# Optimization experiments

Measured on AMD Instinct MI355X. Metric: run time of the kernel, lower is better.

The kernel has to match this reference:

```python
import jax, jax.numpy as jnp
import numpy as np

D_MODEL = 1024
D_FF = 4096
NUM_EXPERTS = 8
TOP_K = 2


def setup_inputs() -> dict:
    key = jax.random.key(0)
    ks = jax.random.split(key, 8)
    s_in = 1.0 / np.sqrt(D_MODEL)
    s_ff = 1.0 / np.sqrt(D_FF)
    x = jax.random.normal(ks[0], (2, 2048, D_MODEL), dtype=jnp.float32)
    Wg = jax.random.uniform(ks[1], (D_MODEL, NUM_EXPERTS), minval=-s_in, maxval=s_in, dtype=jnp.float32)
    bg = jax.random.uniform(ks[2], (NUM_EXPERTS,), minval=-s_in, maxval=s_in, dtype=jnp.float32)
    W1 = jax.random.uniform(ks[3], (NUM_EXPERTS, D_MODEL, D_FF), minval=-s_in, maxval=s_in, dtype=jnp.float32)
    b1 = jax.random.uniform(ks[4], (NUM_EXPERTS, D_FF), minval=-s_in, maxval=s_in, dtype=jnp.float32)
    W2 = jax.random.uniform(ks[5], (NUM_EXPERTS, D_FF, D_MODEL), minval=-s_ff, maxval=s_ff, dtype=jnp.float32)
    b2 = jax.random.uniform(ks[6], (NUM_EXPERTS, D_MODEL), minval=-s_ff, maxval=s_ff, dtype=jnp.float32)
    return {"x": x, "Wg": Wg, "bg": bg, "W1": W1, "b1": b1, "W2": W2, "b2": b2}


def reference(x, Wg, bg, W1, b1, W2, b2):
    # Gating: softmax over experts, top-k, renormalize
    gate_logits = jnp.einsum('bsd,de->bse', x, Wg) + bg
    gate_probs = jax.nn.softmax(gate_logits, axis=-1)
    topk_probs, topk_idx = jax.lax.top_k(gate_probs, TOP_K)
    topk_probs = topk_probs / jnp.sum(topk_probs, axis=-1, keepdims=True)
    # Per-token combine weights over experts [B,S,E] (top-k indices are unique)
    onehot = jax.nn.one_hot(topk_idx, NUM_EXPERTS, dtype=x.dtype)  # [B,S,K,E]
    weights = jnp.einsum('bske,bsk->bse', onehot, topk_probs)
    # Dense per-expert FFN (exact GELU matches torch nn.GELU default)
    h = jnp.einsum('bsd,edf->bsef', x, W1) + b1  # [B,S,E,Dff]
    h = jax.nn.gelu(h, approximate=False)
    y = jnp.einsum('bsef,efd->bsed', h, W2) + b2  # [B,S,E,D]
    return jnp.einsum('bsed,bse->bsd', y, weights)
```

## Files before the change

### kernel.cpp

```cpp
#include <hip/hip_runtime.h>
#include <hip/hip_bf16.h>
#include <math.h>

#define D_MODEL 1024
#define D_FF    4096
#define NE      8
#define NTOK    4096
#define MAXTOK  4096

#define MAXROWS 10240
#define MAXMT   40

typedef __attribute__((ext_vector_type(8))) short short8;
typedef __attribute__((ext_vector_type(4))) float f32x4;

#define WS_CNT     0
#define WS_OFFA    128
#define WS_TOKIDS  1024
#define WS_TOKW    (WS_TOKIDS + NE*MAXTOK*4)
#define WS_ROWTOK  (WS_TOKW + NE*MAXTOK*4)
#define WS_ROWW    (WS_ROWTOK + MAXROWS*4)
#define WS_TOKEXP  (WS_ROWW + MAXROWS*4)

#define WS_H       524288
#define WS_W1T     (WS_H   + (size_t)MAXROWS*D_FF*2)
#define WS_XG      (WS_W1T + (size_t)NE*D_MODEL*D_FF*2)
#define WS_W2T     (WS_XG  + (size_t)MAXROWS*D_MODEL*2)
#define WS_NEED_A  (WS_W2T + (size_t)NE*D_MODEL*D_FF*2)

__device__ __forceinline__ ushort f2b(float v) {
    __hip_bfloat16 b = __float2bfloat16(v);
    return *reinterpret_cast<ushort*>(&b);
}

__device__ __forceinline__ float gelu_f(float v) {
    float z = fabsf(v) * 0.70710678118654752f;
    float t = 1.0f / (1.0f + 0.3275911f * z);
    float p = t * (0.254829592f + t * (-0.284496736f + t * (1.421413741f + t * (-1.453152027f + t * 1.061405429f))));
    float er = 1.0f - p * __expf(-z * z);
    float s = (v >= 0.0f) ? er : -er;
    return 0.5f * v * (1.0f + s);
}

__device__ __forceinline__ int xcd_swz(int orig, int nwg) {
    int q = nwg >> 3, r = nwg & 7;
    int xcd = orig & 7, pos = orig >> 3;
    return (xcd < r ? xcd * (q + 1) : r * (q + 1) + (xcd - r) * q) + pos;
}

__global__ __launch_bounds__(256) void gating_kernel(
    const float* __restrict__ x, const float* __restrict__ Wg, const float* __restrict__ bg,
    int* __restrict__ cnt, int* __restrict__ tok_ids, float* __restrict__ tok_w,
    int* __restrict__ tokexp)
{
    __shared__ float s_wg[D_MODEL * NE];
    int tid = threadIdx.x;
    for (int i = tid; i < D_MODEL * NE; i += 256) s_wg[i] = Wg[i];
    __syncthreads();

    int t = blockIdx.x * 256 + tid;
    float acc[NE];
    #pragma unroll
    for (int e = 0; e < NE; ++e) acc[e] = bg[e];
    const float* xr = x + (size_t)t * D_MODEL;
    for (int d = 0; d < D_MODEL; d += 4) {
        float4 xv = *reinterpret_cast<const float4*>(xr + d);
        #pragma unroll
        for (int e = 0; e < NE; ++e) {
            acc[e] += xv.x * s_wg[(d + 0) * NE + e];
            acc[e] += xv.y * s_wg[(d + 1) * NE + e];
            acc[e] += xv.z * s_wg[(d + 2) * NE + e];
            acc[e] += xv.w * s_wg[(d + 3) * NE + e];
        }
    }
    int i0 = 0;
    #pragma unroll
    for (int e = 1; e < NE; ++e) if (acc[e] > acc[i0]) i0 = e;
    int i1 = (i0 == 0) ? 1 : 0;
    #pragma unroll
    for (int e = 0; e < NE; ++e) if (e != i0 && acc[e] > acc[i1]) i1 = e;
    float e1 = __expf(acc[i1] - acc[i0]);
    float inv = 1.0f / (1.0f + e1);
    float w0 = inv, w1 = e1 * inv;

    int p0 = atomicAdd(&cnt[i0], 1);
    tok_ids[i0 * MAXTOK + p0] = t;  tok_w[i0 * MAXTOK + p0] = w0;
    tokexp[t * 2 + 0] = i0 * MAXTOK + p0;
    int p1 = atomicAdd(&cnt[i1], 1);
    tok_ids[i1 * MAXTOK + p1] = t;  tok_w[i1 * MAXTOK + p1] = w1;
    tokexp[t * 2 + 1] = i1 * MAXTOK + p1;
}

__global__ void scan256_kernel(const int* __restrict__ cnt, int* __restrict__ off) {
    if (threadIdx.x == 0) {
        int acc = 0;
        for (int e = 0; e < NE; ++e) { off[e] = acc; acc += ((cnt[e] + 255) & ~255); }
        off[NE] = acc;
    }
}

__global__ __launch_bounds__(256) void gather_kernel(
    const float* __restrict__ x, const int* __restrict__ cnt, const int* __restrict__ off,
    const int* __restrict__ tok_ids, const float* __restrict__ tok_w,
    ushort* __restrict__ Xg, int* __restrict__ rowtok, float* __restrict__ roww)
{
    int e = blockIdx.y;
    int npad = off[e + 1] - off[e];
    int r0 = blockIdx.x * 128;
    if (r0 >= npad) return;
    int n = cnt[e];
    int base = off[e];
    for (int idx = threadIdx.x; idx < 128 * 128; idx += 256) {
        int r = r0 + (idx >> 7);
        int s = idx & 127;
        int R = base + r;
        int tok = -1;
        float4 v0 = {0, 0, 0, 0}, v1 = {0, 0, 0, 0};
        if (r < n) {
            tok = tok_ids[e * MAXTOK + r];
            const float4* src = (const float4*)(x + (size_t)tok * D_MODEL + s * 8);
            v0 = src[0]; v1 = src[1];
        }
        ushort o[8];
        o[0] = f2b(v0.x); o[1] = f2b(v0.y); o[2] = f2b(v0.z); o[3] = f2b(v0.w);
        o[4] = f2b(v1.x); o[5] = f2b(v1.y); o[6] = f2b(v1.z); o[7] = f2b(v1.w);
        int c = s >> 3, sub = s & 7;
        int ds = sub ^ (R & 7);
        *(uint4*)(Xg + (size_t)R * D_MODEL + c * 64 + ds * 8) = *(const uint4*)o;
        if (s == 0) {
            rowtok[R] = tok;
            roww[R] = (tok >= 0) ? tok_w[e * MAXTOK + r] : 0.0f;
        }
    }
}

__global__ __launch_bounds__(256) void wconv_all(
    const float* __restrict__ W1, const float* __restrict__ W2,
    ushort* __restrict__ W1T, ushort* __restrict__ W2T)
{
    __shared__ float st[64][65];
    int z = blockIdx.y;
    const float* s; ushort* d; int K, N;
    if (z < 8) { s = W1 + (size_t)z * D_MODEL * D_FF;       d = W1T + (size_t)z * D_MODEL * D_FF; K = D_MODEL; N = D_FF; }
    else       { s = W2 + (size_t)(z - 8) * D_FF * D_MODEL; d = W2T + (size_t)(z - 8) * D_FF * D_MODEL; K = D_FF; N = D_MODEL; }
    int nblk = N >> 6;
    int bx = blockIdx.x;
    int n0 = (bx % nblk) * 64;
    int k0 = (bx / nblk) * 64;
    for (int i = threadIdx.x; i < 4096; i += 256) {
        int kr = i >> 6, nc = i & 63;
        st[kr][nc] = s[(size_t)(k0 + kr) * N + n0 + nc];
    }
    __syncthreads();
    int c = k0 >> 6;
    #pragma unroll
    for (int it = 0; it < 2; ++it) {
        int v = threadIdx.x + it * 256;
        int nl = v >> 3, sub = v & 7;
        ushort o[8];
        #pragma unroll
        for (int j = 0; j < 8; ++j) o[j] = f2b(st[sub * 8 + j][nl]);
        int ds = sub ^ ((n0 + nl) & 7);
        *(uint4*)(d + (size_t)(n0 + nl) * K + c * 64 + ds * 8) = *(const uint4*)o;
    }
}


__global__ __launch_bounds__(512, 2) void gemm1_256(
    const ushort* __restrict__ Xg, const ushort* __restrict__ W1T,
    const float* __restrict__ b1, const int* __restrict__ off,
    ushort* __restrict__ H)
{
    __shared__ ushort smem[65536];
    int wid = xcd_swz(blockIdx.x, MAXMT * 16);
    int mt = wid >> 4, nt = wid & 15;
    int row0 = mt << 8;
    if (row0 >= off[NE]) return;
    int e = 0;
    #pragma unroll
    for (int i = 1; i < NE; ++i) if (off[i] <= row0) e = i;
    int nb0 = nt << 8;
    int tid = threadIdx.x;
    int lane = tid & 63, wave = tid >> 6;
    int wr = wave >> 2, wc = wave & 3;

    const ushort* Abase = Xg + (size_t)row0 * D_MODEL;
    const ushort* Bbase = W1T + ((size_t)e * D_FF + nb0) * D_MODEL;

    f32x4 acc[8][4];
    #pragma unroll
    for (int m = 0; m < 8; ++m)
        #pragma unroll
        for (int n = 0; n < 4; ++n)
            acc[m][n] = (f32x4){0.f, 0.f, 0.f, 0.f};

    #define STAGE1(buf, kt) { \
        _Pragma("unroll") \
        for (int r = 0; r < 4; ++r) { \
            int flat = r * 512 + tid; int row_ = flat >> 3, sl = flat & 7; \
            __builtin_amdgcn_global_load_lds((const __attribute__((address_space(1))) void*)(Abase + (size_t)row_ * D_MODEL + (kt) * 64 + sl * 8), \
                (__attribute__((address_space(3))) void*)(smem + (buf) * 16384 + flat * 8), 16, 0, 0); \
            __builtin_amdgcn_global_load_lds((const __attribute__((address_space(1))) void*)(Bbase + (size_t)row_ * D_MODEL + (kt) * 64 + sl * 8), \
                (__attribute__((address_space(3))) void*)(smem + 32768 + (buf) * 16384 + flat * 8), 16, 0, 0); \
        } }

    STAGE1(0, 0);
    __syncthreads();
    for (int kt = 0; kt < 16; ++kt) {
        int cur = kt & 1;
        if (kt + 1 < 16) STAGE1(cur ^ 1, kt + 1);
        const ushort* sAc = smem + cur * 16384;
        const ushort* sBc = smem + 32768 + cur * 16384;
        #pragma unroll
        for (int ks = 0; ks < 2; ++ks) {
            int j = ks * 4 + (lane >> 4);
            short8 b[4];
            #pragma unroll
            for (int n = 0; n < 4; ++n) {
                int brow = wc * 64 + n * 16 + (lane & 15);
                b[n] = *(const short8*)(sBc + brow * 64 + (j ^ (brow & 7)) * 8);
            }
            #pragma unroll
            for (int m = 0; m < 8; ++m) {
                int arow = wr * 128 + m * 16 + (lane & 15);
                short8 a = *(const short8*)(sAc + arow * 64 + (j ^ (arow & 7)) * 8);
                #pragma unroll
                for (int n = 0; n < 4; ++n)
                    acc[m][n] = __builtin_amdgcn_mfma_f32_16x16x32_bf16(a, b[n], acc[m][n], 0, 0, 0);
            }
        }
        __syncthreads();
    }

    const float* b1e = b1 + (size_t)e * D_FF + nb0;
    #pragma unroll
    for (int n = 0; n < 4; ++n) {
        int col = wc * 64 + n * 16 + (lane & 15);
        float bv = b1e[col];
        int gl = col >> 3, el = col & 7;
        #pragma unroll
        for (int m = 0; m < 8; ++m) {
            int rbase = wr * 128 + m * 16 + (lane >> 4) * 4;
            #pragma unroll
            for (int q = 0; q < 4; ++q) {
                int row = rbase + q;
                float v = gelu_f(acc[m][n][q] + bv);
                int g = (gl & ~7) | ((gl ^ row) & 7);
                smem[row * 256 + g * 8 + el] = f2b(v);
            }
        }
    }
    __syncthreads();
    #pragma unroll
    for (int it = 0; it < 16; ++it) {
        int flat = it * 512 + tid;
        int row = flat >> 5, g = flat & 31;
        *(uint4*)(H + (size_t)(row0 + row) * D_FF + nb0 + g * 8) = *(const uint4*)(smem + flat * 8);
    }
}

__global__ __launch_bounds__(512, 2) void gemm2_256(
    const ushort* __restrict__ H, const ushort* __restrict__ W2T,
    const float* __restrict__ b2, const int* __restrict__ off,
    float* __restrict__ Y)
{
    __shared__ ushort smem[65536];
    int wid = xcd_swz(blockIdx.x, MAXMT * 8);
    int nt = wid / (2 * MAXMT);
    int ks = (wid / MAXMT) & 1;
    int mt = wid % MAXMT;
    int row0 = mt << 8;
    if (row0 >= off[NE]) return;
    int e = 0;
    #pragma unroll
    for (int i = 1; i < NE; ++i) if (off[i] <= row0) e = i;
    int nb0 = nt << 8;
    int tid = threadIdx.x;
    int lane = tid & 63, wave = tid >> 6;
    int wr = wave >> 2, wc = wave & 3;
    int kt0 = ks * 32;

    const ushort* Abase = H + (size_t)row0 * D_FF;
    const ushort* Bbase = W2T + ((size_t)e * D_MODEL + nb0) * D_FF;

    f32x4 acc[8][4];
    #pragma unroll
    for (int m = 0; m < 8; ++m)
        #pragma unroll
        for (int n = 0; n < 4; ++n)
            acc[m][n] = (f32x4){0.f, 0.f, 0.f, 0.f};

    #define STAGE2(buf, kt) { \
        _Pragma("unroll") \
        for (int r = 0; r < 4; ++r) { \
            int flat = r * 512 + tid; int row_ = flat >> 3, sl = flat & 7; \
            __builtin_amdgcn_global_load_lds((const __attribute__((address_space(1))) void*)(Abase + (size_t)row_ * D_FF + (kt) * 64 + sl * 8), \
                (__attribute__((address_space(3))) void*)(smem + (buf) * 16384 + flat * 8), 16, 0, 0); \
            __builtin_amdgcn_global_load_lds((const __attribute__((address_space(1))) void*)(Bbase + (size_t)row_ * D_FF + (kt) * 64 + sl * 8), \
                (__attribute__((address_space(3))) void*)(smem + 32768 + (buf) * 16384 + flat * 8), 16, 0, 0); \
        } }

    STAGE2(0, kt0);
    __syncthreads();
    for (int i = 0; i < 32; ++i) {
        int cur = i & 1;
        if (i + 1 < 32) STAGE2(cur ^ 1, kt0 + i + 1);
        const ushort* sAc = smem + cur * 16384;
        const ushort* sBc = smem + 32768 + cur * 16384;
        #pragma unroll
        for (int ksu = 0; ksu < 2; ++ksu) {
            int j = ksu * 4 + (lane >> 4);
            short8 b[4];
            #pragma unroll
            for (int n = 0; n < 4; ++n) {
                int brow = wc * 64 + n * 16 + (lane & 15);
                b[n] = *(const short8*)(sBc + brow * 64 + (j ^ (brow & 7)) * 8);
            }
            #pragma unroll
            for (int m = 0; m < 8; ++m) {
                int arow = wr * 128 + m * 16 + (lane & 15);
                short8 a = *(const short8*)(sAc + arow * 64 + (j ^ (arow & 7)) * 8);
                #pragma unroll
                for (int n = 0; n < 4; ++n)
                    acc[m][n] = __builtin_amdgcn_mfma_f32_16x16x32_bf16(a, b[n], acc[m][n], 0, 0, 0);
            }
        }
        __syncthreads();
    }

    float* Yb = Y + (size_t)ks * MAXROWS * D_MODEL;
    const float* b2e = b2 + (size_t)e * D_MODEL + nb0;
    #pragma unroll
    for (int n = 0; n < 4; ++n) {
        int col = wc * 64 + n * 16 + (lane & 15);
        float bv = (ks == 0) ? b2e[col] : 0.0f;
        #pragma unroll
        for (int m = 0; m < 8; ++m) {
            int rbase = wr * 128 + m * 16 + (lane >> 4) * 4;
            #pragma unroll
            for (int q = 0; q < 4; ++q)
                Yb[(size_t)(row0 + rbase + q) * D_MODEL + nb0 + col] = acc[m][n][q] + bv;
        }
    }
}

__global__ __launch_bounds__(256) void combine_kernel(
    const float* __restrict__ Y, const int* __restrict__ off,
    const int* __restrict__ tokexp, const float* __restrict__ tok_w,
    float* __restrict__ out, int nks)
{
    int t = blockIdx.x;
    int pos0 = tokexp[2 * t], pos1 = tokexp[2 * t + 1];
    int e0 = pos0 >> 12, p0 = pos0 & (MAXTOK - 1);
    int e1 = pos1 >> 12, p1 = pos1 & (MAXTOK - 1);
    size_t R0 = off[e0] + p0, R1 = off[e1] + p1;
    float w0 = tok_w[pos0], w1 = tok_w[pos1];
    int c = threadIdx.x * 4;
    float y0x = 0, y0y = 0, y0z = 0, y0w = 0;
    float y1x = 0, y1y = 0, y1z = 0, y1w = 0;
    for (int s = 0; s < nks; ++s) {
        const float* Ys = Y + (size_t)s * MAXROWS * D_MODEL;
        float4 a = *(const float4*)(Ys + R0 * D_MODEL + c);
        float4 b = *(const float4*)(Ys + R1 * D_MODEL + c);
        y0x += a.x; y0y += a.y; y0z += a.z; y0w += a.w;
        y1x += b.x; y1y += b.y; y1z += b.z; y1w += b.w;
    }
    float4 o;
    o.x = w0 * y0x + w1 * y1x;
    o.y = w0 * y0y + w1 * y1y;
    o.z = w0 * y0z + w1 * y1z;
    o.w = w0 * y0w + w1 * y1w;
    *(float4*)(out + (size_t)t * D_MODEL + c) = o;
}

#define TM      32
#define FFC     128
#define KSTEP   64

__global__ __launch_bounds__(512) void ffn_kernel(
    const float* __restrict__ x,
    const float* __restrict__ W1, const float* __restrict__ b1,
    const float* __restrict__ W2, const float* __restrict__ b2,
    const int* __restrict__ cnt, const int* __restrict__ tok_ids, const float* __restrict__ tok_w,
    float* __restrict__ out)
{
    int e = blockIdx.y;
    int n = cnt[e];
    int t0 = blockIdx.x * TM;
    if (t0 >= n) return;
    int tid = threadIdx.x;

    __shared__ int   s_tok[TM];
    __shared__ float s_w[TM];
    __shared__ float s_x[TM][KSTEP];
    __shared__ float s_w1[KSTEP][FFC];
    __shared__ float s_h[TM][FFC];

    if (tid < TM) {
        int idx = t0 + tid;
        s_tok[tid] = (idx < n) ? tok_ids[e * MAXTOK + idx] : -1;
        s_w[tid]   = (idx < n) ? tok_w[e * MAXTOK + idx] : 0.0f;
    }
    __syncthreads();

    float acc[TM][2];
    #pragma unroll
    for (int i = 0; i < TM; ++i) { acc[i][0] = 0.0f; acc[i][1] = 0.0f; }

    const float* W1e = W1 + (size_t)e * D_MODEL * D_FF;
    const float* W2e = W2 + (size_t)e * D_FF * D_MODEL;
    const float* b1e = b1 + (size_t)e * D_FF;

    int ffl = (tid & 63) * 2;
    int g   = tid >> 6;

    int fb0 = blockIdx.z * (D_FF / 2);
    for (int fb = fb0; fb < fb0 + D_FF / 2; fb += FFC) {
        float bv0 = b1e[fb + ffl], bv1 = b1e[fb + ffl + 1];
        float hacc[4][2];
        #pragma unroll
        for (int j = 0; j < 4; ++j) { hacc[j][0] = bv0; hacc[j][1] = bv1; }

        for (int kb = 0; kb < D_MODEL; kb += KSTEP) {
            #pragma unroll
            for (int r = 0; r < 4; ++r) {
                int i = tid + 512 * r;
                int row = i >> 6, col = i & 63;
                int tok = s_tok[row];
                s_x[row][col] = (tok >= 0) ? x[(size_t)tok * D_MODEL + kb + col] : 0.0f;
            }
            #pragma unroll
            for (int r = 0; r < 16; ++r) {
                int i = tid + 512 * r;
                int row = i >> 7, col = i & 127;
                s_w1[row][col] = W1e[(size_t)(kb + row) * D_FF + fb + col];
            }
            __syncthreads();
            #pragma unroll 8
            for (int kk = 0; kk < KSTEP; ++kk) {
                float2 wv = *reinterpret_cast<const float2*>(&s_w1[kk][ffl]);
                #pragma unroll
                for (int j = 0; j < 4; ++j) {
                    float xv = s_x[g * 4 + j][kk];
                    hacc[j][0] += xv * wv.x;
                    hacc[j][1] += xv * wv.y;
                }
            }
            __syncthreads();
        }
        #pragma unroll
        for (int j = 0; j < 4; ++j) {
            #pragma unroll
            for (int p = 0; p < 2; ++p) {
                float v = hacc[j][p];
                v = 0.5f * v * (1.0f + erff(v * 0.70710678118654752f));
                s_h[g * 4 + j][ffl + p] = v;
            }
        }
        __syncthreads();
        for (int ff = 0; ff < FFC; ++ff) {
            const float* w2row = W2e + (size_t)(fb + ff) * D_MODEL;
            float wc0 = w2row[tid], wc1 = w2row[tid + 512];
            #pragma unroll
            for (int tt = 0; tt < TM; ++tt) {
                float hv = s_h[tt][ff];
                acc[tt][0] += hv * wc0;
                acc[tt][1] += hv * wc1;
            }
        }
        __syncthreads();
    }

    float bc0 = b2[(size_t)e * D_MODEL + tid];
    float bc1 = b2[(size_t)e * D_MODEL + tid + 512];
    if (blockIdx.z != 0) { bc0 = 0.0f; bc1 = 0.0f; }
    #pragma unroll
    for (int tt = 0; tt < TM; ++tt) {
        int tok = s_tok[tt];
        if (tok >= 0) {
            float w = s_w[tt];
            atomicAdd(&out[(size_t)tok * D_MODEL + tid],       w * (acc[tt][0] + bc0));
            atomicAdd(&out[(size_t)tok * D_MODEL + tid + 512], w * (acc[tt][1] + bc1));
        }
    }
}

extern "C" void kernel_launch(void* const* d_in, const int* in_sizes, int n_in,
                              void* d_out, int out_size, void* d_ws, size_t ws_size,
                              hipStream_t stream) {
    const float* x  = (const float*)d_in[0];
    const float* Wg = (const float*)d_in[1];
    const float* bg = (const float*)d_in[2];
    const float* W1 = (const float*)d_in[3];
    const float* b1 = (const float*)d_in[4];
    const float* W2 = (const float*)d_in[5];
    const float* b2 = (const float*)d_in[6];
    float* out = (float*)d_out;

    char* ws = (char*)d_ws;
    int*    cnt     = (int*)(ws + WS_CNT);
    int*    offp    = (int*)(ws + WS_OFFA);
    int*    tok_ids = (int*)(ws + WS_TOKIDS);
    float*  tok_w   = (float*)(ws + WS_TOKW);
    int*    rowtok  = (int*)(ws + WS_ROWTOK);
    float*  roww    = (float*)(ws + WS_ROWW);
    int*    tokexp  = (int*)(ws + WS_TOKEXP);

    hipMemsetAsync(cnt, 0, NE * sizeof(int), stream);
    gating_kernel<<<NTOK / 256, 256, 0, stream>>>(x, Wg, bg, cnt, tok_ids, tok_w, tokexp);

    if (ws_size >= WS_NEED_A) {
        ushort* Hb  = (ushort*)(ws + WS_H);
        ushort* W1T = (ushort*)(ws + WS_W1T);
        ushort* Xg  = (ushort*)(ws + WS_XG);
        ushort* W2T = (ushort*)(ws + WS_W2T);
        float*  Y   = (float*)(ws + WS_W1T);
        const int nks = 2;

        scan256_kernel<<<1, 64, 0, stream>>>(cnt, offp);
        wconv_all<<<dim3(1024, 16), 256, 0, stream>>>(W1, W2, W1T, W2T);
        gather_kernel<<<dim3(32, NE), 256, 0, stream>>>(x, cnt, offp, tok_ids, tok_w, Xg, rowtok, roww);
        gemm1_256<<<MAXMT * 16, 512, 0, stream>>>(Xg, W1T, b1, offp, Hb);
        gemm2_256<<<MAXMT * 8, 512, 0, stream>>>(Hb, W2T, b2, offp, Y);
        combine_kernel<<<NTOK, 256, 0, stream>>>(Y, offp, tokexp, tok_w, out, nks);
    } else {
        hipMemsetAsync(out, 0, (size_t)out_size * sizeof(float), stream);
        dim3 grid(MAXTOK / TM, NE, 2);
        ffn_kernel<<<grid, 512, 0, stream>>>(x, W1, b1, W2, b2, cnt, tok_ids, tok_w, out);
    }
}
```

Measured before the change: 459.6 us.

## Deepen GEMM prefetch to four-stage K=32 ring with explicit vmcnt waits

Both expert GEMM kernels move from a two-buffer K=64 pipeline with full __syncthreads per step to a four-slot ring of K=32 tiles, with three tiles prefetched ahead. Each step waits only on its own tile using s_waitcnt vmcnt plus s_barrier, with a new swizzle for the half-width rows. The weight-conversion kernel also switches its loads to float4. The aim is to keep more global-to-LDS traffic in flight and shorten barrier stalls, at the cost of twice as many barriers and hand-counted vmcnt values that must exactly match the number of issued loads.

```diff
diff --git a/kernel.cpp b/kernel.cpp
--- a/kernel.cpp
+++ b/kernel.cpp
@@ -147,9 +147,12 @@
     int bx = blockIdx.x;
     int n0 = (bx % nblk) * 64;
     int k0 = (bx / nblk) * 64;
-    for (int i = threadIdx.x; i < 4096; i += 256) {
-        int kr = i >> 6, nc = i & 63;
-        st[kr][nc] = s[(size_t)(k0 + kr) * N + n0 + nc];
+    #pragma unroll
+    for (int it = 0; it < 4; ++it) {
+        int v = threadIdx.x + it * 256;
+        int kr = v >> 4, nc = (v & 15) * 4;
+        float4 t = *(const float4*)(s + (size_t)(k0 + kr) * N + n0 + nc);
+        st[kr][nc + 0] = t.x; st[kr][nc + 1] = t.y; st[kr][nc + 2] = t.z; st[kr][nc + 3] = t.w;
     }
     __syncthreads();
     int c = k0 >> 6;
@@ -165,6 +168,43 @@
     }
 }
 
+
+#define STG(kabs, Abase, Bbase, LD) { \
+    _Pragma("unroll") \
+    for (int l = 0; l < 2; ++l) { \
+        int flat = l * 512 + tid; int r_ = flat >> 2, jp = flat & 3; \
+        int jL = jp ^ (r_ & 3); \
+        int pA = ((((kabs) & 1) * 4 + jL) ^ (r_ & 7)) * 8; \
+        int gcol = (((kabs) >> 1) * 64) + pA; \
+        __builtin_amdgcn_global_load_lds((const __attribute__((address_space(1))) void*)((Abase) + (size_t)r_ * (LD) + gcol), \
+            (__attribute__((address_space(3))) void*)(smem + ((kabs) & 3) * 8192 + flat * 8), 16, 0, 0); \
+        __builtin_amdgcn_global_load_lds((const __attribute__((address_space(1))) void*)((Bbase) + (size_t)r_ * (LD) + gcol), \
+            (__attribute__((address_space(3))) void*)(smem + 32768 + ((kabs) & 3) * 8192 + flat * 8), 16, 0, 0); \
+    } }
+
+#define CMP(kabs) { \
+    const ushort* As_ = smem + ((kabs) & 3) * 8192; \
+    const ushort* Bs_ = smem + 32768 + ((kabs) & 3) * 8192; \
+    short8 b[4]; \
+    _Pragma("unroll") \
+    for (int n = 0; n < 4; ++n) { \
+        int br = wc * 64 + n * 16 + l15; \
+        b[n] = *(const short8*)(Bs_ + br * 32 + (jj ^ (br & 3)) * 8); \
+    } \
+    _Pragma("unroll") \
+    for (int m = 0; m < 8; ++m) { \
+        int ar = wr * 128 + m * 16 + l15; \
+        short8 a = *(const short8*)(As_ + ar * 32 + (jj ^ (ar & 3)) * 8); \
+        _Pragma("unroll") \
+        for (int n = 0; n < 4; ++n) \
+            acc[m][n] = __builtin_amdgcn_mfma_f32_16x16x32_bf16(a, b[n], acc[m][n], 0, 0, 0); \
+    } }
+
+#define VMB(nn) { \
+    asm volatile("s_waitcnt vmcnt(" #nn ")" ::: "memory"); \
+    asm volatile("s_barrier" ::: "memory"); }
+
+#define BAR() asm volatile("s_barrier" ::: "memory")
 
 __global__ __launch_bounds__(512, 2) void gemm1_256(
     const ushort* __restrict__ Xg, const ushort* __restrict__ W1T,
@@ -183,6 +223,7 @@
     int tid = threadIdx.x;
     int lane = tid & 63, wave = tid >> 6;
     int wr = wave >> 2, wc = wave & 3;
+    int jj = lane >> 4, l15 = lane & 15;
 
     const ushort* Abase = Xg + (size_t)row0 * D_MODEL;
     const ushort* Bbase = W1T + ((size_t)e * D_FF + nb0) * D_MODEL;
@@ -194,53 +235,29 @@
         for (int n = 0; n < 4; ++n)
             acc[m][n] = (f32x4){0.f, 0.f, 0.f, 0.f};
 
-    #define STAGE1(buf, kt) { \
-        _Pragma("unroll") \
-        for (int r = 0; r < 4; ++r) { \
-            int flat = r * 512 + tid; int row_ = flat >> 3, sl = flat & 7; \
-            __builtin_amdgcn_global_load_lds((const __attribute__((address_space(1))) void*)(Abase + (size_t)row_ * D_MODEL + (kt) * 64 + sl * 8), \
-                (__attribute__((address_space(3))) void*)(smem + (buf) * 16384 + flat * 8), 16, 0, 0); \
-            __builtin_amdgcn_global_load_lds((const __attribute__((address_space(1))) void*)(Bbase + (size_t)row_ * D_MODEL + (kt) * 64 + sl * 8), \
-                (__attribute__((address_space(3))) void*)(smem + 32768 + (buf) * 16384 + flat * 8), 16, 0, 0); \
-        } }
-
-    STAGE1(0, 0);
+    STG(0, Abase, Bbase, D_MODEL);
+    STG(1, Abase, Bbase, D_MODEL);
+    STG(2, Abase, Bbase, D_MODEL);
+    for (int kt = 0; kt < 29; ++kt) {
+        STG(kt + 3, Abase, Bbase, D_MODEL);
+        VMB(12);
+        CMP(kt);
+        BAR();
+    }
+    VMB(8);  CMP(29); BAR();
+    VMB(4);  CMP(30); BAR();
+    VMB(0);  CMP(31);
     __syncthreads();
-    for (int kt = 0; kt < 16; ++kt) {
-        int cur = kt & 1;
-        if (kt + 1 < 16) STAGE1(cur ^ 1, kt + 1);
-        const ushort* sAc = smem + cur * 16384;
-        const ushort* sBc = smem + 32768 + cur * 16384;
-        #pragma unroll
-        for (int ks = 0; ks < 2; ++ks) {
-            int j = ks * 4 + (lane >> 4);
-            short8 b[4];
-            #pragma unroll
-            for (int n = 0; n < 4; ++n) {
-                int brow = wc * 64 + n * 16 + (lane & 15);
-                b[n] = *(const short8*)(sBc + brow * 64 + (j ^ (brow & 7)) * 8);
-            }
-            #pragma unroll
-            for (int m = 0; m < 8; ++m) {
-                int arow = wr * 128 + m * 16 + (lane & 15);
-                short8 a = *(const short8*)(sAc + arow * 64 + (j ^ (arow & 7)) * 8);
-                #pragma unroll
-                for (int n = 0; n < 4; ++n)
-                    acc[m][n] = __builtin_amdgcn_mfma_f32_16x16x32_bf16(a, b[n], acc[m][n], 0, 0, 0);
-            }
-        }
-        __syncthreads();
-    }
 
     const float* b1e = b1 + (size_t)e * D_FF + nb0;
     #pragma unroll
     for (int n = 0; n < 4; ++n) {
-        int col = wc * 64 + n * 16 + (lane & 15);
+        int col = wc * 64 + n * 16 + l15;
         float bv = b1e[col];
         int gl = col >> 3, el = col & 7;
         #pragma unroll
         for (int m = 0; m < 8; ++m) {
-            int rbase = wr * 128 + m * 16 + (lane >> 4) * 4;
+            int rbase = wr * 128 + m * 16 + jj * 4;
             #pragma unroll
             for (int q = 0; q < 4; ++q) {
                 int row = rbase + q;
@@ -278,7 +295,8 @@
     int tid = threadIdx.x;
     int lane = tid & 63, wave = tid >> 6;
     int wr = wave >> 2, wc = wave & 3;
-    int kt0 = ks * 32;
+    int jj = lane >> 4, l15 = lane & 15;
+    int kb = ks * 64;
 
     const ushort* Abase = H + (size_t)row0 * D_FF;
     const ushort* Bbase = W2T + ((size_t)e * D_MODEL + nb0) * D_FF;
@@ -290,53 +308,28 @@
         for (int n = 0; n < 4; ++n)
             acc[m][n] = (f32x4){0.f, 0.f, 0.f, 0.f};
 
-    #define STAGE2(buf, kt) { \
-        _Pragma("unroll") \
-        for (int r = 0; r < 4; ++r) { \
-            int flat = r * 512 + tid; int row_ = flat >> 3, sl = flat & 7; \
-            __builtin_amdgcn_global_load_lds((const __attribute__((address_space(1))) void*)(Abase + (size_t)row_ * D_FF + (kt) * 64 + sl * 8), \
-                (__attribute__((address_space(3))) void*)(smem + (buf) * 16384 + flat * 8), 16, 0, 0); \
-            __builtin_amdgcn_global_load_lds((const __attribute__((address_space(1))) void*)(Bbase + (size_t)row_ * D_FF + (kt) * 64 + sl * 8), \
-                (__attribute__((address_space(3))) void*)(smem + 32768 + (buf) * 16384 + flat * 8), 16, 0, 0); \
-        } }
-
-    STAGE2(0, kt0);
-    __syncthreads();
-    for (int i = 0; i < 32; ++i) {
-        int cur = i & 1;
-        if (i + 1 < 32) STAGE2(cur ^ 1, kt0 + i + 1);
-        const ushort* sAc = smem + cur * 16384;
-        const ushort* sBc = smem + 32768 + cur * 16384;
-        #pragma unroll
-        for (int ksu = 0; ksu < 2; ++ksu) {
-            int j = ksu * 4 + (lane >> 4);
-            short8 b[4];
-            #pragma unroll
-            for (int n = 0; n < 4; ++n) {
-                int brow = wc * 64 + n * 16 + (lane & 15);
-                b[n] = *(const short8*)(sBc + brow * 64 + (j ^ (brow & 7)) * 8);
-            }
-            #pragma unroll
-            for (int m = 0; m < 8; ++m) {
-                int arow = wr * 128 + m * 16 + (lane & 15);
-                short8 a = *(const short8*)(sAc + arow * 64 + (j ^ (arow & 7)) * 8);
-                #pragma unroll
-                for (int n = 0; n < 4; ++n)
-                    acc[m][n] = __builtin_amdgcn_mfma_f32_16x16x32_bf16(a, b[n], acc[m][n], 0, 0, 0);
-            }
-        }
-        __syncthreads();
-    }
+    STG(kb + 0, Abase, Bbase, D_FF);
+    STG(kb + 1, Abase, Bbase, D_FF);
+    STG(kb + 2, Abase, Bbase, D_FF);
+    for (int lt = 0; lt < 61; ++lt) {
+        STG(kb + lt + 3, Abase, Bbase, D_FF);
+        VMB(12);
+        CMP(kb + lt);
+        BAR();
+    }
+    VMB(8);  CMP(kb + 61); BAR();
+    VMB(4);  CMP(kb + 62); BAR();
+    VMB(0);  CMP(kb + 63);
 
     float* Yb = Y + (size_t)ks * MAXROWS * D_MODEL;
     const float* b2e = b2 + (size_t)e * D_MODEL + nb0;
     #pragma unroll
     for (int n = 0; n < 4; ++n) {
-        int col = wc * 64 + n * 16 + (lane & 15);
+        int col = wc * 64 + n * 16 + l15;
         float bv = (ks == 0) ? b2e[col] : 0.0f;
         #pragma unroll
         for (int m = 0; m < 8; ++m) {
-            int rbase = wr * 128 + m * 16 + (lane >> 4) * 4;
+            int rbase = wr * 128 + m * 16 + jj * 4;
             #pragma unroll
             for (int q = 0; q < 4; ++q)
                 Yb[(size_t)(row0 + rbase + q) * D_MODEL + nb0 + col] = acc[m][n][q] + bv;
```

Measured after the change: 492.7 us. 7.2% more time.
